# Performance work log

Hardware: AMD Instinct MI355X
Metric: run time of the kernel (lower is better)

The kernel has to match this reference:

```python
import jax, jax.numpy as jnp
import numpy as np

# TISA RBF basis (helpers l2_dist / rbf_basis in the repo): f_i(d) = a_i * exp(-|b_i| * (d - c_i)^2)

def setup_inputs() -> dict:
    key = jax.random.key(0)
    k = jax.random.split(key, 8)
    B, L, H, D, S, F = 2, 2048, 8, 64, 2, 5
    qs = jax.random.normal(k[0], (B, L, H, D), dtype=jnp.float32)
    ks = jax.random.normal(k[1], (B, L, H, D), dtype=jnp.float32)
    vs = jax.random.normal(k[2], (B, L, H, D), dtype=jnp.float32)
    qs_s = jax.random.uniform(k[3], (B, L, S), dtype=jnp.float32)
    ks_s = jax.random.uniform(k[4], (B, L, S), dtype=jnp.float32)
    a = jax.random.uniform(k[5], (H * F,), dtype=jnp.float32)
    b = jax.random.uniform(k[6], (H * F,), dtype=jnp.float32)
    c = jax.random.normal(k[7], (H * F,), dtype=jnp.float32) * 0.5
    return {"qs": qs, "ks": ks, "vs": vs, "qs_s": qs_s, "ks_s": ks_s, "a": a, "b": b, "c": c}


def _tisa_attention(qs, ks, vs, qs_s, ks_s, a, b, c):
    B, Q, H, D = qs.shape
    F = a.size // H
    aH, bH, cH = (p.reshape(H, F) for p in (a, b, c))
    # pairwise euclidean distance between query and key locations: [B, Q, K]
    diff = qs_s[:, :, None, :] - ks_s[:, None, :, :]
    d = jnp.sqrt(jnp.sum(diff * diff, axis=-1))
    d_ = d[:, None]  # [B, 1, Q, K] broadcast over heads
    # RBF bias summed over F basis functions (small fixed F -> python sum avoids B,H,F,Q,K blowup)
    bias = sum(
        aH[:, f][None, :, None, None]
        * jnp.exp(-jnp.abs(bH[:, f])[None, :, None, None] * (d_ - cH[:, f][None, :, None, None]) ** 2)
        for f in range(F)
    )  # [B, H, Q, K]
    scale = 1.0 / jnp.sqrt(jnp.asarray(D, dtype=qs.dtype))
    scores = jnp.einsum('bqhd,bkhd->bhqk', qs * scale, ks) + bias
    attn = jax.nn.softmax(scores, axis=-1)
    return jnp.einsum('bhqk,bkhd->bqhd', attn, vs)


def reference(qs, ks, vs, qs_s, ks_s, a, b, c):
    # Matches scan_tisa_biased_attention: online-softmax chunking is mathematically
    # identical to a single stable softmax over the full key axis.
    return _tisa_attention(qs, ks, vs, qs_s, ks_s, a, b, c)
```

## Files before the change

kernel.cpp:

```cpp
#include <hip/hip_runtime.h>
#include <cmath>

typedef _Float16 half8 __attribute__((ext_vector_type(8)));
typedef _Float16 half2v __attribute__((ext_vector_type(2)));
typedef float f32x4 __attribute__((ext_vector_type(4)));
typedef float f32x2 __attribute__((ext_vector_type(2)));

#define B_ 2
#define L_ 2048
#define H_ 8
#define D_ 64
#define S_ 2
#define F_ 5
#define LUTN 2048
#define LSCALE 1448.1547f
#define LOG2E 1.44269504f
#define QSC (0.125f * LOG2E)

#define QOFF 0
#define KOFF 2097152
#define VOFF 4194304
#define SOFFH 6291456
#define WS_NEED 12615680

#define OFF_K 0
#define OFF_V 16384
#define OFF_P 32768
#define OFF_LUT 53248
#define OFF_KSS 61456
#define ARENA_SZ 62480
#define SLOTF (16 * 68 + 16)

#define GLOBAL_LOAD_LDS16(g, l)                                                  \
  __builtin_amdgcn_global_load_lds((const __attribute__((address_space(1))) void*)(g), \
                                   (__attribute__((address_space(3))) void*)(l), 16, 0, 0)

#define FAST_SQRT(x) __builtin_amdgcn_sqrtf(x)

__global__ __launch_bounds__(256, 4)
void tisa_preproc(const float* __restrict__ qs, const float* __restrict__ ks,
                  const float* __restrict__ vs, const float* __restrict__ ks_s,
                  _Float16* __restrict__ wsh) {
  __shared__ _Float16 Vl[64 * 72];
  const int t = threadIdx.x;
  const int u = blockIdx.x & 31;
  const int bh = blockIdx.x >> 5;
  const size_t base = ((size_t)(bh >> 3) * L_ + (size_t)u * 64) * (H_ * D_) + (size_t)(bh & 7) * D_;

#pragma unroll
  for (int jj = 0; jj < 2; ++jj) {
    int id = t * 2 + jj;
    int row = id >> 3, c = id & 7;
    const float* src = qs + base + (size_t)row * 512 + c * 8;
    f32x4 x0 = ((const f32x4*)src)[0], x1 = ((const f32x4*)src)[1];
    half8 hh;
#pragma unroll
    for (int k = 0; k < 4; ++k) { hh[k] = (_Float16)(x0[k] * QSC); hh[k + 4] = (_Float16)(x1[k] * QSC); }
    *(half8*)&wsh[QOFF + ((size_t)bh * 32 + u) * 4096 + row * 64 + (c ^ (row & 7)) * 8] = hh;
  }
#pragma unroll
  for (int jj = 0; jj < 2; ++jj) {
    int id = t * 2 + jj;
    int tile = id >> 8, row = (id >> 3) & 31, c = id & 7;
    const float* src = ks + base + (size_t)(tile * 32 + row) * 512 + c * 8;
    f32x4 x0 = ((const f32x4*)src)[0], x1 = ((const f32x4*)src)[1];
    half8 hh;
#pragma unroll
    for (int k = 0; k < 4; ++k) { hh[k] = (_Float16)x0[k]; hh[k + 4] = (_Float16)x1[k]; }
    *(half8*)&wsh[KOFF + ((size_t)bh * 64 + u * 2 + tile) * 2048 + row * 64 + (c ^ (row & 7)) * 8] = hh;
  }
  if ((bh & 7) == 0 && t < 32) {
    const int b = bh >> 3;
    const float* src = ks_s + ((size_t)b * L_ + u * 64) * 2 + t * 4;
    float* dst = (float*)(wsh + SOFFH) + ((size_t)b * L_ + u * 64) * 2 + t * 4;
    f32x4 x = *(const f32x4*)src;
    x *= LSCALE;
    *(f32x4*)dst = x;
  }
  {
    int key = t >> 2, d0 = (t & 3) * 16;
    const float* src = vs + base + (size_t)key * 512 + d0;
    f32x4 a0 = ((const f32x4*)src)[0], a1 = ((const f32x4*)src)[1];
    f32x4 a2 = ((const f32x4*)src)[2], a3 = ((const f32x4*)src)[3];
    half8 h0, h1;
#pragma unroll
    for (int k = 0; k < 4; ++k) {
      h0[k] = (_Float16)a0[k]; h0[k + 4] = (_Float16)a1[k];
      h1[k] = (_Float16)a2[k]; h1[k + 4] = (_Float16)a3[k];
    }
    *(half8*)&Vl[key * 72 + d0] = h0;
    *(half8*)&Vl[key * 72 + d0 + 8] = h1;
  }
  __syncthreads();
#pragma unroll
  for (int jj = 0; jj < 2; ++jj) {
    int id = t * 2 + jj;
    int tile = id >> 8, s = (id >> 3) & 31, cp = id & 7;
    int d = 2 * s + (cp >> 2), kb = (cp & 3) * 8;
    half8 hh;
#pragma unroll
    for (int j = 0; j < 8; ++j) hh[j] = Vl[(tile * 32 + kb + j) * 72 + d];
    *(half8*)&wsh[VOFF + ((size_t)bh * 64 + u * 2 + tile) * 2048 + s * 64 + (cp ^ (s & 7)) * 8] = hh;
  }
}

__global__ __launch_bounds__(1024, 8)
void tisa_attn_main(const float* __restrict__ qs_s, const float* __restrict__ ap,
                    const float* __restrict__ bp, const float* __restrict__ cp,
                    const _Float16* __restrict__ wsh, float* __restrict__ out) {
  __shared__ __align__(16) char arena[ARENA_SZ];
  float* LUT = (float*)(arena + OFF_LUT);

  const int t = threadIdx.x;
  const int lane = t & 63;
  const int w = t >> 6;
  const int g = w >> 2;
  const int qw = w & 3;
  const int t2 = t & 255;
  const int quad = lane >> 4;
  const int l16 = lane & 15;

  const int qt = blockIdx.x & 31;
  const int bh = blockIdx.x >> 5;
  const int h = bh & 7;
  const int b = bh >> 3;
  const int q0 = qt * 64;

  {
    float af[F_], nb[F_], cf[F_];
#pragma unroll
    for (int f = 0; f < F_; ++f) {
      af[f] = ap[h * F_ + f];
      nb[f] = -fabsf(bp[h * F_ + f]);
      cf[f] = cp[h * F_ + f];
    }
    for (int i = t; i <= LUTN; i += 1024) {
      float d = ((float)i + 0.5f) * (1.0f / LSCALE);
      float s = 0.f;
#pragma unroll
      for (int f = 0; f < F_; ++f) {
        float e = d - cf[f];
        s += af[f] * __expf(nb[f] * (e * e));
      }
      LUT[i] = (s - 8.0f) * LOG2E;
    }
  }

  float qx[4], qy[4];
#pragma unroll
  for (int r = 0; r < 4; ++r) {
    int qrow = q0 + qw * 16 + quad * 4 + r;
    qx[r] = qs_s[((size_t)b * L_ + qrow) * 2 + 0] * LSCALE;
    qy[r] = qs_s[((size_t)b * L_ + qrow) * 2 + 1] * LSCALE;
  }

  const _Float16* Qt = wsh + QOFF + ((size_t)bh * 32 + qt) * 4096;
  const _Float16* Kbh = wsh + KOFF + (size_t)bh * 64 * 2048;
  const _Float16* Vbh = wsh + VOFF + (size_t)bh * 64 * 2048;
  const float* wsS = (const float*)(wsh + SOFFH);

  if (w < 8)
    GLOBAL_LOAD_LDS16(Qt + w * 512 + lane * 8, arena + OFF_K + w * 1024);
  __syncthreads();

  half8 qA[2];
#pragma unroll
  for (int kb = 0; kb < 2; ++kb)
    qA[kb] = *(const half8*)(arena + OFF_K + (qw * 16 + l16) * 128 +
                             ((kb * 4 + quad) ^ (l16 & 7)) * 16);

  f32x4 oc[4];
#pragma unroll
  for (int df = 0; df < 4; ++df) oc[df] = (f32x4){0.f, 0.f, 0.f, 0.f};
  f32x4 lsacc = (f32x4){0.f, 0.f, 0.f, 0.f};
  half8 onesv;
#pragma unroll
  for (int j = 0; j < 8; ++j) onesv[j] = (_Float16)1.0f;

  const _Float16* ksrc = Kbh + (size_t)(g * 16) * 2048 + t2 * 8;
  const _Float16* vsrc = Vbh + (size_t)(g * 16) * 2048 + t2 * 8;
  const f32x2* ssrc = (const f32x2*)(wsS + ((size_t)b * L_ + g * 512) * 2);
  char* kdst = arena + OFF_K + g * 4096 + qw * 1024;
  char* vdst = arena + OFF_V + g * 4096 + qw * 1024;
  f32x2* kssG = (f32x2*)(arena + OFF_KSS + g * 256);
  _Float16* Pw = (_Float16*)(arena + OFF_P + w * 1280 + quad * 320 + l16 * 2);

  for (int it = 0; it < 16; ++it) {
    __syncthreads();
    GLOBAL_LOAD_LDS16(ksrc, kdst);
    GLOBAL_LOAD_LDS16(vsrc, vdst);
    ksrc += 2048; vsrc += 2048;
    if (t2 < 32) kssG[t2] = ssrc[t2];
    ssrc += 32;
    __syncthreads();

    f32x4 acc[2];
#pragma unroll
    for (int nf = 0; nf < 2; ++nf) {
      f32x4 a = (f32x4){0.f, 0.f, 0.f, 0.f};
#pragma unroll
      for (int kb = 0; kb < 2; ++kb) {
        half8 kf = *(const half8*)(arena + OFF_K + g * 4096 + (nf * 16 + l16) * 128 +
                                   ((kb * 4 + quad) ^ (l16 & 7)) * 16);
        a = __builtin_amdgcn_mfma_f32_16x16x32_f16(qA[kb], kf, a, 0, 0, 0);
      }
      acc[nf] = a;
    }

#pragma unroll
    for (int nf = 0; nf < 2; ++nf) {
      f32x2 kc = kssG[nf * 16 + l16];
#pragma unroll
      for (int r = 0; r < 4; ++r) {
        float dx = qx[r] - kc.x, dy = qy[r] - kc.y;
        float tt = FAST_SQRT(fmaf(dx, dx, dy * dy));
        int ii = (int)tt;
        float p = __builtin_amdgcn_exp2f(acc[nf][r] + LUT[ii]);
        acc[nf][r] = p;
        Pw[r * 40 + nf * 16] = (_Float16)p;
      }
    }

    half8 pa = *(const half8*)(arena + OFF_P + w * 1280 + l16 * 80 + quad * 16);
    lsacc = __builtin_amdgcn_mfma_f32_16x16x32_f16(pa, onesv, lsacc, 0, 0, 0);
#pragma unroll
    for (int df = 0; df < 4; ++df) {
      half8 vf = *(const half8*)(arena + OFF_V + g * 4096 + (l16 >> 1) * 128 + df * 1024 +
                                 ((((l16 & 1) * 4 + quad) ^ ((l16 >> 1) & 7)) * 16));
      oc[df] = __builtin_amdgcn_mfma_f32_16x16x32_f16(pa, vf, oc[df], 0, 0, 0);
    }
  }

  float lred[4];
#pragma unroll
  for (int r = 0; r < 4; ++r) lred[r] = lsacc[r];
  __syncthreads();
  float* slots = (float*)arena;
  if (g >= 2) {
    float* sl = slots + ((g - 2) * 4 + qw) * SLOTF;
#pragma unroll
    for (int df = 0; df < 4; ++df)
#pragma unroll
      for (int r = 0; r < 4; ++r)
        sl[(quad * 4 + r) * 68 + df * 16 + l16] = oc[df][r];
    if (l16 == 0) {
#pragma unroll
      for (int r = 0; r < 4; ++r) sl[16 * 68 + quad * 4 + r] = lred[r];
    }
  }
  __syncthreads();
  if (g < 2) {
    float* sl = slots + (g * 4 + qw) * SLOTF;
#pragma unroll
    for (int df = 0; df < 4; ++df)
#pragma unroll
      for (int r = 0; r < 4; ++r)
        oc[df][r] += sl[(quad * 4 + r) * 68 + df * 16 + l16];
#pragma unroll
    for (int r = 0; r < 4; ++r) lred[r] += sl[16 * 68 + quad * 4 + r];
  }
  if (g == 1) {
    float* sl = slots + (4 + qw) * SLOTF;
#pragma unroll
    for (int df = 0; df < 4; ++df)
#pragma unroll
      for (int r = 0; r < 4; ++r)
        sl[(quad * 4 + r) * 68 + df * 16 + l16] = oc[df][r];
    if (l16 == 0) {
#pragma unroll
      for (int r = 0; r < 4; ++r) sl[16 * 68 + quad * 4 + r] = lred[r];
    }
  }
  __syncthreads();
  if (g == 0) {
    float* sl = slots + (4 + qw) * SLOTF;
    float inv_l[4];
#pragma unroll
    for (int r = 0; r < 4; ++r)
      inv_l[r] = 1.f / (lred[r] + sl[16 * 68 + quad * 4 + r]);
#pragma unroll
    for (int df = 0; df < 4; ++df)
#pragma unroll
      for (int r = 0; r < 4; ++r) {
        int qrow = q0 + qw * 16 + quad * 4 + r;
        float v = oc[df][r] + sl[(quad * 4 + r) * 68 + df * 16 + l16];
        out[((size_t)(b * L_ + qrow)) * (H_ * D_) + h * D_ + df * 16 + l16] = v * inv_l[r];
      }
  }
}

#define KSTR 72
#define PH 72
#define FLUTN 512
#define FLSCALE 362.03867f
__global__ __launch_bounds__(512, 4)
void tisa_attn_fallback(const float* __restrict__ qs, const float* __restrict__ ks,
                        const float* __restrict__ vs, const float* __restrict__ qs_s,
                        const float* __restrict__ ks_s, const float* __restrict__ ap,
                        const float* __restrict__ bp, const float* __restrict__ cp,
                        float* __restrict__ out) {
  __shared__ _Float16 Ks[2][64 * KSTR];
  __shared__ _Float16 VT[2][D_ * KSTR];
  __shared__ _Float16 Pf[8][16 * PH];
  __shared__ float kss2[2][64 * 2];
  __shared__ f32x2 LUT2s[FLUTN + 1];
  __shared__ float comb[4][16][64];
  __shared__ float combl[4][16];

  const int t = threadIdx.x;
  const int lane = t & 63;
  const int w = t >> 6;
  const int g = w >> 2;
  const int qw = w & 3;
  const int t2 = t & 255;
  const int quad = lane >> 4;
  const int l16 = lane & 15;
  const int qt = blockIdx.x & 31;
  const int bh = blockIdx.x >> 5;
  const int h = bh & 7;
  const int b = bh >> 3;
  const int q0 = qt * 64;

  float af[F_], nb[F_], cf[F_];
#pragma unroll
  for (int f = 0; f < F_; ++f) {
    af[f] = ap[h * F_ + f];
    nb[f] = -fabsf(bp[h * F_ + f]);
    cf[f] = cp[h * F_ + f];
  }
  for (int i = t; i <= FLUTN; i += 512) {
    float d0 = (float)i * (1.0f / FLSCALE), d1 = (float)(i + 1) * (1.0f / FLSCALE);
    float s0 = 0.f, s1 = 0.f;
#pragma unroll
    for (int f = 0; f < F_; ++f) {
      float e0 = d0 - cf[f], e1 = d1 - cf[f];
      s0 += af[f] * __expf(nb[f] * (e0 * e0));
      s1 += af[f] * __expf(nb[f] * (e1 * e1));
    }
    LUT2s[i] = (f32x2){s0 - 8.0f, s1 - 8.0f};
  }
  float qx[4], qy[4];
#pragma unroll
  for (int r = 0; r < 4; ++r) {
    int qrow = q0 + qw * 16 + quad * 4 + r;
    qx[r] = qs_s[(b * L_ + qrow) * S_ + 0];
    qy[r] = qs_s[(b * L_ + qrow) * S_ + 1];
  }
  if (t < 256) {
    const int row = t >> 2, dc = (t & 3) * 16;
    const float* src = qs + (((size_t)(b * L_ + q0 + row)) * H_ + h) * D_ + dc;
    const f32x4* s4 = (const f32x4*)src;
    f32x4 v0 = s4[0], v1 = s4[1], v2 = s4[2], v3 = s4[3];
    half8 w0, w1;
#pragma unroll
    for (int u = 0; u < 4; ++u) {
      w0[u] = (_Float16)(v0[u] * 0.125f); w0[u + 4] = (_Float16)(v1[u] * 0.125f);
      w1[u] = (_Float16)(v2[u] * 0.125f); w1[u + 4] = (_Float16)(v3[u] * 0.125f);
    }
    *(half8*)&Ks[0][row * KSTR + dc] = w0;
    *(half8*)&Ks[0][row * KSTR + dc + 8] = w1;
  }
  __syncthreads();
  half8 qA[2];
#pragma unroll
  for (int kb = 0; kb < 2; ++kb)
    qA[kb] = *(const half8*)&Ks[0][(qw * 16 + l16) * KSTR + kb * 32 + quad * 8];
  f32x4 oc[4];
#pragma unroll
  for (int df = 0; df < 4; ++df) oc[df] = (f32x4){0.f, 0.f, 0.f, 0.f};
  float l_r[4] = {0.f, 0.f, 0.f, 0.f};

  for (int it = 0; it < 16; ++it) {
    const int k0 = (g * 16 + it) * 64;
    __syncthreads();
    {
      const int row = t2 >> 2, dc = (t2 & 3) * 16;
      const float* src = ks + (((size_t)(b * L_ + k0 + row)) * H_ + h) * D_ + dc;
      const f32x4* s4 = (const f32x4*)src;
      f32x4 v0 = s4[0], v1 = s4[1], v2 = s4[2], v3 = s4[3];
      half8 w0, w1;
#pragma unroll
      for (int u = 0; u < 4; ++u) {
        w0[u] = (_Float16)v0[u]; w0[u + 4] = (_Float16)v1[u];
        w1[u] = (_Float16)v2[u]; w1[u + 4] = (_Float16)v3[u];
      }
      *(half8*)&Ks[g][row * KSTR + dc] = w0;
      *(half8*)&Ks[g][row * KSTR + dc + 8] = w1;
    }
    {
      const int kk = (t2 & 31) * 2, dg = (t2 >> 5) * 8;
      const float* s0 = vs + (((size_t)(b * L_ + k0 + kk)) * H_ + h) * D_ + dg;
      const float* s1 = s0 + H_ * D_;
      f32x4 a0 = ((const f32x4*)s0)[0], a1 = ((const f32x4*)s0)[1];
      f32x4 b0 = ((const f32x4*)s1)[0], b1 = ((const f32x4*)s1)[1];
#pragma unroll
      for (int u = 0; u < 4; ++u) {
        half2v p0 = {(_Float16)a0[u], (_Float16)b0[u]};
        *(half2v*)&VT[g][(dg + u) * KSTR + kk] = p0;
        half2v p1 = {(_Float16)a1[u], (_Float16)b1[u]};
        *(half2v*)&VT[g][(dg + 4 + u) * KSTR + kk] = p1;
      }
    }
    if (t2 < 128) kss2[g][t2] = ks_s[((size_t)(b * L_) + k0 + (t2 >> 1)) * S_ + (t2 & 1)];
    __syncthreads();
    f32x4 acc[4];
#pragma unroll
    for (int nf = 0; nf < 4; ++nf) {
      f32x4 a = (f32x4){0.f, 0.f, 0.f, 0.f};
#pragma unroll
      for (int kb = 0; kb < 2; ++kb) {
        half8 kf = *(const half8*)&Ks[g][(nf * 16 + l16) * KSTR + kb * 32 + quad * 8];
        a = __builtin_amdgcn_mfma_f32_16x16x32_f16(qA[kb], kf, a, 0, 0, 0);
      }
      acc[nf] = a;
    }
#pragma unroll
    for (int nf = 0; nf < 4; ++nf) {
      float kx = kss2[g][(nf * 16 + l16) * 2 + 0];
      float ky = kss2[g][(nf * 16 + l16) * 2 + 1];
#pragma unroll
      for (int r = 0; r < 4; ++r) {
        float dx = qx[r] - kx, dy = qy[r] - ky;
        float dist = FAST_SQRT(fmaf(dx, dx, dy * dy));
        float tt = dist * FLSCALE;
        int ii = (int)tt;
        float fr = tt - (float)ii;
        f32x2 lh = LUT2s[ii];
        float p = __expf(acc[nf][r] + fmaf(fr, lh.y - lh.x, lh.x));
        acc[nf][r] = p;
      }
    }
#pragma unroll
    for (int r = 0; r < 4; ++r)
      l_r[r] += (acc[0][r] + acc[1][r]) + (acc[2][r] + acc[3][r]);
#pragma unroll
    for (int nf = 0; nf < 4; ++nf)
#pragma unroll
      for (int r = 0; r < 4; ++r)
        Pf[w][(quad * 4 + r) * PH + nf * 16 + l16] = (_Float16)acc[nf][r];
#pragma unroll
    for (int kb = 0; kb < 2; ++kb) {
      half8 pa = *(const half8*)&Pf[w][l16 * PH + kb * 32 + quad * 8];
#pragma unroll
      for (int df = 0; df < 4; ++df) {
        half8 vf = *(const half8*)&VT[g][(df * 16 + l16) * KSTR + kb * 32 + quad * 8];
        oc[df] = __builtin_amdgcn_mfma_f32_16x16x32_f16(pa, vf, oc[df], 0, 0, 0);
      }
    }
  }
  __syncthreads();
  float lred[4];
#pragma unroll
  for (int r = 0; r < 4; ++r) {
    float s = l_r[r];
    s += __shfl_xor(s, 1); s += __shfl_xor(s, 2);
    s += __shfl_xor(s, 4); s += __shfl_xor(s, 8);
    lred[r] = s;
  }
  if (g == 1) {
#pragma unroll
    for (int df = 0; df < 4; ++df)
#pragma unroll
      for (int r = 0; r < 4; ++r)
        comb[qw][quad * 4 + r][df * 16 + l16] = oc[df][r];
    if (l16 == 0) {
#pragma unroll
      for (int r = 0; r < 4; ++r) combl[qw][quad * 4 + r] = lred[r];
    }
  }
  __syncthreads();
  if (g == 0) {
    float inv_l[4];
#pragma unroll
    for (int r = 0; r < 4; ++r)
      inv_l[r] = 1.f / (lred[r] + combl[qw][quad * 4 + r]);
#pragma unroll
    for (int df = 0; df < 4; ++df)
#pragma unroll
      for (int r = 0; r < 4; ++r) {
        int qrow = q0 + qw * 16 + quad * 4 + r;
        float v = oc[df][r] + comb[qw][quad * 4 + r][df * 16 + l16];
        out[(((size_t)(b * L_ + qrow)) * H_ + h) * D_ + df * 16 + l16] = v * inv_l[r];
      }
  }
}

extern "C" void kernel_launch(void* const* d_in, const int* in_sizes, int n_in,
                              void* d_out, int out_size, void* d_ws, size_t ws_size,
                              hipStream_t stream) {
  const float* qs = (const float*)d_in[0];
  const float* ks = (const float*)d_in[1];
  const float* vs = (const float*)d_in[2];
  const float* qs_s = (const float*)d_in[3];
  const float* ks_s = (const float*)d_in[4];
  const float* ap = (const float*)d_in[5];
  const float* bp = (const float*)d_in[6];
  const float* cp = (const float*)d_in[7];
  float* out = (float*)d_out;

  if (ws_size >= (size_t)WS_NEED) {
    _Float16* wsh = (_Float16*)d_ws;
    tisa_preproc<<<dim3(512), dim3(256), 0, stream>>>(qs, ks, vs, ks_s, wsh);
    tisa_attn_main<<<dim3(512), dim3(1024), 0, stream>>>(qs_s, ap, bp, cp, wsh, out);
  } else {
    tisa_attn_fallback<<<dim3(512), dim3(512), 0, stream>>>(qs, ks, vs, qs_s, ks_s, ap, bp, cp, out);
  }
}
```

Baseline: 134.8 us.

## Transpose QK MFMA so P is written as packed half4 and key coords load from global

Swaps the MFMA operand order so each lane holds scores for one query row and four consecutive keys. The P tile can then be written to LDS as one packed half4 store instead of four scalar half stores. Each lane now needs only one query coordinate, and key coordinates are read directly from global memory as vector loads, which removes the LDS staging array for key coordinates. The cost is extra global loads per iteration, issued before the barrier, in place of a shared LDS broadcast.

```diff
diff --git a/kernel.cpp b/kernel.cpp
--- a/kernel.cpp
+++ b/kernel.cpp
@@ -2,6 +2,7 @@
 #include <cmath>
 
 typedef _Float16 half8 __attribute__((ext_vector_type(8)));
+typedef _Float16 half4 __attribute__((ext_vector_type(4)));
 typedef _Float16 half2v __attribute__((ext_vector_type(2)));
 typedef float f32x4 __attribute__((ext_vector_type(4)));
 typedef float f32x2 __attribute__((ext_vector_type(2)));
@@ -27,8 +28,7 @@
 #define OFF_V 16384
 #define OFF_P 32768
 #define OFF_LUT 53248
-#define OFF_KSS 61456
-#define ARENA_SZ 62480
+#define ARENA_SZ 61456
 #define SLOTF (16 * 68 + 16)
 
 #define GLOBAL_LOAD_LDS16(g, l)                                                  \
@@ -95,12 +95,12 @@
 #pragma unroll
   for (int jj = 0; jj < 2; ++jj) {
     int id = t * 2 + jj;
-    int tile = id >> 8, s = (id >> 3) & 31, cp = id & 7;
-    int d = 2 * s + (cp >> 2), kb = (cp & 3) * 8;
+    int tile = id >> 8, s = (id >> 3) & 31, cp2 = id & 7;
+    int d = 2 * s + (cp2 >> 2), kb = (cp2 & 3) * 8;
     half8 hh;
 #pragma unroll
     for (int j = 0; j < 8; ++j) hh[j] = Vl[(tile * 32 + kb + j) * 72 + d];
-    *(half8*)&wsh[VOFF + ((size_t)bh * 64 + u * 2 + tile) * 2048 + s * 64 + (cp ^ (s & 7)) * 8] = hh;
+    *(half8*)&wsh[VOFF + ((size_t)bh * 64 + u * 2 + tile) * 2048 + s * 64 + (cp2 ^ (s & 7)) * 8] = hh;
   }
 }
 
@@ -146,13 +146,8 @@
     }
   }
 
-  float qx[4], qy[4];
-#pragma unroll
-  for (int r = 0; r < 4; ++r) {
-    int qrow = q0 + qw * 16 + quad * 4 + r;
-    qx[r] = qs_s[((size_t)b * L_ + qrow) * 2 + 0] * LSCALE;
-    qy[r] = qs_s[((size_t)b * L_ + qrow) * 2 + 1] * LSCALE;
-  }
+  const float qx = qs_s[((size_t)b * L_ + q0 + qw * 16 + l16) * 2 + 0] * LSCALE;
+  const float qy = qs_s[((size_t)b * L_ + q0 + qw * 16 + l16) * 2 + 1] * LSCALE;
 
   const _Float16* Qt = wsh + QOFF + ((size_t)bh * 32 + qt) * 4096;
   const _Float16* Kbh = wsh + KOFF + (size_t)bh * 64 * 2048;
@@ -179,19 +174,22 @@
 
   const _Float16* ksrc = Kbh + (size_t)(g * 16) * 2048 + t2 * 8;
   const _Float16* vsrc = Vbh + (size_t)(g * 16) * 2048 + t2 * 8;
-  const f32x2* ssrc = (const f32x2*)(wsS + ((size_t)b * L_ + g * 512) * 2);
+  const float* sbase = wsS + ((size_t)b * L_ + g * 512 + quad * 4) * 2;
   char* kdst = arena + OFF_K + g * 4096 + qw * 1024;
   char* vdst = arena + OFF_V + g * 4096 + qw * 1024;
-  f32x2* kssG = (f32x2*)(arena + OFF_KSS + g * 256);
-  _Float16* Pw = (_Float16*)(arena + OFF_P + w * 1280 + quad * 320 + l16 * 2);
+  char* Pp = arena + OFF_P + w * 1280 + l16 * 80 + quad * 8;
 
   for (int it = 0; it < 16; ++it) {
+    const float* sit = sbase + it * 64;
+    f32x4 c01a = *(const f32x4*)(sit);
+    f32x4 c23a = *(const f32x4*)(sit + 4);
+    f32x4 c01b = *(const f32x4*)(sit + 32);
+    f32x4 c23b = *(const f32x4*)(sit + 36);
+
     __syncthreads();
     GLOBAL_LOAD_LDS16(ksrc, kdst);
     GLOBAL_LOAD_LDS16(vsrc, vdst);
     ksrc += 2048; vsrc += 2048;
-    if (t2 < 32) kssG[t2] = ssrc[t2];
-    ssrc += 32;
     __syncthreads();
 
     f32x4 acc[2];
@@ -202,23 +200,28 @@
       for (int kb = 0; kb < 2; ++kb) {
         half8 kf = *(const half8*)(arena + OFF_K + g * 4096 + (nf * 16 + l16) * 128 +
                                    ((kb * 4 + quad) ^ (l16 & 7)) * 16);
-        a = __builtin_amdgcn_mfma_f32_16x16x32_f16(qA[kb], kf, a, 0, 0, 0);
+        a = __builtin_amdgcn_mfma_f32_16x16x32_f16(kf, qA[kb], a, 0, 0, 0);
       }
       acc[nf] = a;
     }
 
 #pragma unroll
     for (int nf = 0; nf < 2; ++nf) {
-      f32x2 kc = kssG[nf * 16 + l16];
+      f32x4 cA = (nf == 0) ? c01a : c01b;
+      f32x4 cB = (nf == 0) ? c23a : c23b;
+      float kxr[4] = {cA.x, cA.z, cB.x, cB.z};
+      float kyr[4] = {cA.y, cA.w, cB.y, cB.w};
+      half4 pv;
 #pragma unroll
       for (int r = 0; r < 4; ++r) {
-        float dx = qx[r] - kc.x, dy = qy[r] - kc.y;
+        float dx = qx - kxr[r], dy = qy - kyr[r];
         float tt = FAST_SQRT(fmaf(dx, dx, dy * dy));
         int ii = (int)tt;
         float p = __builtin_amdgcn_exp2f(acc[nf][r] + LUT[ii]);
         acc[nf][r] = p;
-        Pw[r * 40 + nf * 16] = (_Float16)p;
-      }
+        pv[r] = (_Float16)p;
+      }
+      *(half4*)(Pp + nf * 32) = pv;
     }
 
     half8 pa = *(const half8*)(arena + OFF_P + w * 1280 + l16 * 80 + quad * 16);
```

After: 154.4 us. 14.5% more time.
